# Optimization experiments

Hardware: AMD Instinct MI355X
Metric: run time of the kernel (lower is better)

The kernel has to match this reference:

```python
import jax, jax.numpy as jnp
import numpy as np

H = 2048
FF = 5504
N_HEADS = 16
HEAD_DIM = H // N_HEADS
EPS = 1.1920929e-07  # torch.finfo(float32).eps, F.rms_norm default
M_TOTAL = 4096


def _rms_norm(x, w):
    # x: [m, H], w: [H]
    var = jnp.mean(jnp.square(x), axis=-1, keepdims=True)
    return x * jax.lax.rsqrt(var + EPS) * w


def _routed_gemm(h, W, s):
    # rows [0:s) use W[0], rows [s:) use W[1]; split is static (Python int)
    return jnp.concatenate([h[:s] @ W[0], h[s:] @ W[1]], axis=0)


def _sdpa_seg(q, k, v):
    # q,k,v: [m, H] -> full (non-causal) attention over the segment
    m = q.shape[0]
    q = q.reshape(m, N_HEADS, HEAD_DIM)
    k = k.reshape(m, N_HEADS, HEAD_DIM)
    v = v.reshape(m, N_HEADS, HEAD_DIM)
    scale = 1.0 / jnp.sqrt(jnp.asarray(HEAD_DIM, q.dtype))
    scores = jnp.einsum('qhd,khd->hqk', q, k) * scale  # [nh, m, m]
    p = jax.nn.softmax(scores, axis=-1)
    out = jnp.einsum('hqk,khd->qhd', p, v)
    return out.reshape(m, H)


def setup_inputs() -> dict:
    key = jax.random.key(0)
    ks = jax.random.split(key, 5)
    return {
        'x': jax.random.normal(ks[0], (M_TOTAL, H), dtype=jnp.float32),
        'W_qkv': jax.random.normal(ks[1], (2, H, 3 * H), dtype=jnp.float32) * 0.02,
        'W_o': jax.random.normal(ks[2], (2, H, H), dtype=jnp.float32) * 0.02,
        'W_gu': jax.random.normal(ks[3], (2, H, 2 * FF), dtype=jnp.float32) * 0.02,
        'W_d': jax.random.normal(ks[4], (2, FF, H), dtype=jnp.float32) * 0.02,
        'ln1': jnp.ones((2, H), dtype=jnp.float32),
        'ln2': jnp.ones((2, H), dtype=jnp.float32),
        'split_point': 2048,
    }


def reference(x, W_qkv, W_o, W_gu, W_d, ln1, ln2, split_point):
    s = int(split_point)
    M = x.shape[0]

    def per_model(fn2, x, *stacked):
        # apply fn(seg, *per_model_weights) on [0:s) with index 0, [s:) with index 1
        if s == 0:
            return fn2(x, *(w[1] for w in stacked))
        if s == M:
            return fn2(x, *(w[0] for w in stacked))
        a = fn2(x[:s], *(w[0] for w in stacked))
        b = fn2(x[s:], *(w[1] for w in stacked))
        return jnp.concatenate([a, b], axis=0)

    # attention
    h = per_model(_rms_norm, x, ln1)
    qkv = _routed_gemm(h, W_qkv, s)
    q, k, v = jnp.split(qkv, 3, axis=-1)
    if s == 0 or s == M:
        attn = _sdpa_seg(q, k, v)
    else:
        attn = jnp.concatenate([
            _sdpa_seg(q[:s], k[:s], v[:s]),
            _sdpa_seg(q[s:], k[s:], v[s:]),
        ], axis=0)
    x = x + _routed_gemm(attn, W_o, s)

    # MLP (SwiGLU)
    h = per_model(_rms_norm, x, ln2)
    gu = _routed_gemm(h, W_gu, s)
    gate, up = jnp.split(gu, 2, axis=-1)
    h_mlp = jax.nn.silu(gate) * up
    x = x + _routed_gemm(h_mlp, W_d, s)
    return x
```

## Files before the change

kernel.cpp:

```cpp
#include <hip/hip_runtime.h>

typedef short bf16x8 __attribute__((ext_vector_type(8)));
typedef float f32x4  __attribute__((ext_vector_type(4)));
typedef float fvec4  __attribute__((ext_vector_type(4)));
typedef unsigned short u16;
typedef unsigned int u32;
typedef u32 u32x4 __attribute__((ext_vector_type(4)));
typedef u16 u16x8 __attribute__((ext_vector_type(8)));

#define MFMA16(a,b,c) __builtin_amdgcn_mfma_f32_16x16x32_bf16((a),(b),(c),0,0,0)

__device__ __forceinline__ u16 f2bf(float f){
  u32 u = __float_as_uint(f);
  u32 r = (u + 0x7fffu + ((u >> 16) & 1u)) >> 16;
  return (u16)r;
}
__device__ __forceinline__ float bf2f(u16 v){
  return __uint_as_float(((u32)v) << 16);
}
__device__ __forceinline__ void gload_lds16(const void* g, void* l){
  __builtin_amdgcn_global_load_lds((const __attribute__((address_space(1))) void*)g,
                                   (__attribute__((address_space(3))) void*)l, 16, 0, 0);
}

__global__ __launch_bounds__(256) void rmsnorm_kernel(const float* __restrict__ x,
    const float* __restrict__ lnw, const int* __restrict__ splitp, u16* __restrict__ out)
{
  const int row = blockIdx.x, tid = threadIdx.x;
  const float* xr = x + (size_t)row*2048 + tid*8;
  fvec4 v0 = *(const fvec4*)xr;
  fvec4 v1 = *(const fvec4*)(xr + 4);
  float ss = v0[0]*v0[0] + v0[1]*v0[1] + v0[2]*v0[2] + v0[3]*v0[3]
           + v1[0]*v1[0] + v1[1]*v1[1] + v1[2]*v1[2] + v1[3]*v1[3];
  #pragma unroll
  for (int off=32; off; off>>=1) ss += __shfl_xor(ss, off, 64);
  __shared__ float red[4];
  if ((tid & 63) == 0) red[tid>>6] = ss;
  __syncthreads();
  float tot = red[0] + red[1] + red[2] + red[3];
  float rs = rsqrtf(tot * (1.0f/2048.0f) + 1.1920929e-07f);
  int model = (row >= splitp[0]) ? 1 : 0;
  const float* wr = lnw + model*2048 + tid*8;
  fvec4 w0 = *(const fvec4*)wr, w1 = *(const fvec4*)(wr+4);
  u32x4 pk;
  #pragma unroll
  for (int e=0;e<2;++e){
    pk[e]   = (u32)f2bf(v0[2*e]*rs*w0[2*e]) | ((u32)f2bf(v0[2*e+1]*rs*w0[2*e+1]) << 16);
    pk[2+e] = (u32)f2bf(v1[2*e]*rs*w1[2*e]) | ((u32)f2bf(v1[2*e+1]*rs*w1[2*e+1]) << 16);
  }
  *(u32x4*)(out + (size_t)row*2048 + tid*8) = pk;
}

__global__ __launch_bounds__(256) void transpose_w(const float* __restrict__ W,
    u16* __restrict__ Wt, int K, int N)
{
  __shared__ float t[32][33];
  const int n0 = blockIdx.x * 32, k0 = blockIdx.y * 32;
  const float* Wm = W + (size_t)blockIdx.z * K * N;
  u16* Wtm = Wt + (size_t)blockIdx.z * K * N;
  const int tx = threadIdx.x & 31, ty = threadIdx.x >> 5;
  #pragma unroll
  for (int p=0;p<4;++p){
    int k = ty + p*8;
    t[k][tx] = Wm[(size_t)(k0 + k) * N + n0 + tx];
  }
  __syncthreads();
  #pragma unroll
  for (int p=0;p<4;++p){
    int n = ty + p*8;
    Wtm[(size_t)(n0 + n) * K + k0 + tx] = f2bf(t[tx][n]);
  }
}

template<int RESID>
__global__ __launch_bounds__(256) void gemm_routed(
    const u16* __restrict__ A, int lda, const u16* __restrict__ Wt,
    int N, int K, const int* __restrict__ splitp,
    u16* __restrict__ outB, float* __restrict__ outF, const float* __restrict__ res)
{
  __shared__ char Asm[8192];
  __shared__ char Bsm[8192];
  const int tid = threadIdx.x;
  const int w = tid >> 6, l = tid & 63;
  const int ln = l & 15, g = l >> 4;
  const int wm = w >> 1, wn = w & 1;
  const int row0 = blockIdx.x * 128;
  const int n0 = blockIdx.y * 128;
  const int model = (row0 >= splitp[0]) ? 1 : 0;
  const u16* B = Wt + (size_t)model * N * K;

  f32x4 acc[4][4];
  #pragma unroll
  for (int i=0;i<4;++i)
    #pragma unroll
    for (int j=0;j<4;++j) acc[i][j] = f32x4{0.f,0.f,0.f,0.f};

  int arow[2], aj[2];
  #pragma unroll
  for (int i=0;i<2;++i){
    int lin = (w*2+i)*1024 + l*16;
    int r_ = lin >> 6;
    int s_ = (lin >> 4) & 3;
    arow[i] = r_;
    aj[i] = s_ ^ (r_ & 3);
  }

  const int nt = K / 32;
  for (int kt = 0; kt < nt; ++kt){
    __syncthreads();
    #pragma unroll
    for (int i=0;i<2;++i){
      const u16* srcA = A + (size_t)(row0 + arow[i]) * lda + kt*32 + aj[i]*8;
      gload_lds16(srcA, Asm + (w*2+i)*1024);
      const u16* srcB = B + (size_t)(n0 + arow[i]) * K + kt*32 + aj[i]*8;
      gload_lds16(srcB, Bsm + (w*2+i)*1024);
    }
    __syncthreads();

    bf16x8 a[4], b[4];
    #pragma unroll
    for (int mf=0;mf<4;++mf){
      int r_ = wm*64 + mf*16 + ln;
      a[mf] = *(const bf16x8*)(Asm + r_*64 + (((g ^ (r_&3)) & 3) << 4));
    }
    #pragma unroll
    for (int nf=0;nf<4;++nf){
      int r_ = wn*64 + nf*16 + ln;
      b[nf] = *(const bf16x8*)(Bsm + r_*64 + (((g ^ (r_&3)) & 3) << 4));
    }
    #pragma unroll
    for (int mf=0;mf<4;++mf)
      #pragma unroll
      for (int nf=0;nf<4;++nf)
        acc[mf][nf] = MFMA16(a[mf], b[nf], acc[mf][nf]);
  }

  #pragma unroll
  for (int mf=0;mf<4;++mf){
    #pragma unroll
    for (int nf=0;nf<4;++nf){
      #pragma unroll
      for (int r=0;r<4;++r){
        int row = row0 + wm*64 + mf*16 + g*4 + r;
        int col = n0 + wn*64 + nf*16 + ln;
        size_t off = (size_t)row * N + col;
        float v = acc[mf][nf][r];
        if (RESID) outF[off] = v + res[off];
        else       outB[off] = f2bf(v);
      }
    }
  }
}

__global__ __launch_bounds__(256) void attn_kernel(const u16* __restrict__ qkv,
                                                   u16* __restrict__ out)
{
  __shared__ char Ksm[2][8192];
  __shared__ char Vsm[2][8192];
  __shared__ char Psm[4][1024];
  const int tid = threadIdx.x;
  const int w = tid >> 6, l = tid & 63;
  const int ln = l & 15, g = l >> 4;
  const int qt = blockIdx.x, h = blockIdx.y, seg = blockIdx.z;
  const int srow = seg * 2048;
  const float scale = 0.08838834764831845f;

  const int qrow = srow + qt*64 + w*16 + ln;
  bf16x8 qf[4];
  #pragma unroll
  for (int c=0;c<4;++c)
    qf[c] = *(const bf16x8*)(qkv + (size_t)qrow*6144 + h*128 + c*32 + g*8);

  f32x4 oacc[8];
  #pragma unroll
  for (int i=0;i<8;++i) oacc[i] = f32x4{0.f,0.f,0.f,0.f};
  float m[4]    = {-1e30f,-1e30f,-1e30f,-1e30f};
  float lsum[4] = {0.f,0.f,0.f,0.f};

  int kkv[2], ks[2];
  #pragma unroll
  for (int i=0;i<2;++i){
    int lin = (w*2+i)*1024 + l*16;
    int kv = lin >> 8;
    int sp = (lin >> 4) & 15;
    kkv[i] = kv;
    ks[i] = sp ^ (kv & 15);
  }
  const int vkv = tid >> 3, vd0 = (tid & 7) * 16;

  bf16x8 vreg0, vreg1;
  auto stage = [&](int kv0, int buf){
    #pragma unroll
    for (int i=0;i<2;++i){
      const u16* src = qkv + (size_t)(srow + kv0 + kkv[i]) * 6144 + 2048 + h*128 + ks[i]*8;
      gload_lds16(src, Ksm[buf] + (w*2+i)*1024);
    }
    const u16* vs = qkv + (size_t)(srow + kv0 + vkv) * 6144 + 4096 + h*128 + vd0;
    vreg0 = *(const bf16x8*)vs;
    vreg1 = *(const bf16x8*)(vs + 8);
  };
  auto writeV = [&](int buf){
    #pragma unroll
    for (int e=0;e<16;++e){
      int d = vd0 + e;
      u16 val = (u16)((e<8) ? vreg0[e] : vreg1[e-8]);
      int byte = d*64 + ((((vkv>>3) ^ (d&3)) & 3) << 4) + ((vkv & 7) << 1);
      *(u16*)(Vsm[buf] + byte) = val;
    }
  };

  stage(0, 0);
  writeV(0);
  __syncthreads();

  for (int t=0; t<64; ++t){
    int cur = t & 1, nxt = cur ^ 1;
    if (t+1 < 64) stage((t+1)*32, nxt);

    f32x4 s0 = f32x4{0.f,0.f,0.f,0.f}, s1 = f32x4{0.f,0.f,0.f,0.f};
    #pragma unroll
    for (int c=0;c<4;++c){
      int sl = c*4 + g;
      int c0 = ln;
      bf16x8 k0 = *(const bf16x8*)(Ksm[cur] + c0*256 + (((sl ^ (c0&15)) & 15) << 4));
      s0 = MFMA16(qf[c], k0, s0);
      int c1 = 16 + ln;
      bf16x8 k1 = *(const bf16x8*)(Ksm[cur] + c1*256 + (((sl ^ (c1&15)) & 15) << 4));
      s1 = MFMA16(qf[c], k1, s1);
    }
    float mx[4], f_[4];
    #pragma unroll
    for (int r=0;r<4;++r){
      s0[r] *= scale; s1[r] *= scale;
      mx[r] = fmaxf(s0[r], s1[r]);
    }
    #pragma unroll
    for (int off=1; off<16; off<<=1){
      #pragma unroll
      for (int r=0;r<4;++r) mx[r] = fmaxf(mx[r], __shfl_xor(mx[r], off, 64));
    }
    #pragma unroll
    for (int r=0;r<4;++r){
      float mn = fmaxf(m[r], mx[r]);
      f_[r] = __expf(m[r] - mn);
      m[r] = mn;
      lsum[r] *= f_[r];
    }
    #pragma unroll
    for (int r=0;r<4;++r){
      float p0 = __expf(s0[r] - m[r]);
      float p1 = __expf(s1[r] - m[r]);
      lsum[r] += p0 + p1;
      int qq = g*4 + r;
      int c0 = ln, c1 = 16 + ln;
      *(u16*)(Psm[w] + qq*64 + ((((c0>>3) ^ (qq&3)) & 3) << 4) + ((c0&7)<<1)) = f2bf(p0);
      *(u16*)(Psm[w] + qq*64 + ((((c1>>3) ^ (qq&3)) & 3) << 4) + ((c1&7)<<1)) = f2bf(p1);
    }
    {
      int srcl = (ln >> 2) << 4;
      float F0 = __shfl(f_[0], srcl, 64);
      float F1 = __shfl(f_[1], srcl, 64);
      float F2 = __shfl(f_[2], srcl, 64);
      float F3 = __shfl(f_[3], srcl, 64);
      int rr = ln & 3;
      float fc = (rr==0) ? F0 : (rr==1) ? F1 : (rr==2) ? F2 : F3;
      #pragma unroll
      for (int mc=0;mc<8;++mc){
        #pragma unroll
        for (int r=0;r<4;++r) oacc[mc][r] *= fc;
      }
    }
    bf16x8 pf = *(const bf16x8*)(Psm[w] + ln*64 + (((g ^ (ln&3)) & 3) << 4));
    #pragma unroll
    for (int mc=0;mc<8;++mc){
      int d = mc*16 + ln;
      bf16x8 vf = *(const bf16x8*)(Vsm[cur] + d*64 + (((g ^ (d&3)) & 3) << 4));
      oacc[mc] = MFMA16(vf, pf, oacc[mc]);
    }
    if (t+1 < 64) writeV(nxt);
    __syncthreads();
  }

  #pragma unroll
  for (int off=1; off<16; off<<=1){
    #pragma unroll
    for (int r=0;r<4;++r) lsum[r] += __shfl_xor(lsum[r], off, 64);
  }
  int srcl = (ln >> 2) << 4;
  float L0 = __shfl(lsum[0], srcl, 64);
  float L1 = __shfl(lsum[1], srcl, 64);
  float L2 = __shfl(lsum[2], srcl, 64);
  float L3 = __shfl(lsum[3], srcl, 64);
  int rr = ln & 3;
  float Lc = (rr==0) ? L0 : (rr==1) ? L1 : (rr==2) ? L2 : L3;
  float linv = 1.0f / Lc;
  const int orow = srow + qt*64 + w*16 + ln;
  #pragma unroll
  for (int mc=0;mc<8;++mc){
    #pragma unroll
    for (int r=0;r<4;++r){
      int d = mc*16 + g*4 + r;
      out[(size_t)orow*2048 + h*128 + d] = f2bf(oacc[mc][r] * linv);
    }
  }
}

__global__ __launch_bounds__(256) void silu_kernel(const u16* __restrict__ gu,
                                                   u16* __restrict__ hm)
{
  int u = blockIdx.x*256 + threadIdx.x;
  if (u >= 4096*688) return;
  int row = u / 688;
  int j = (u - row*688) * 8;
  const u16* gp = gu + (size_t)row*11008 + j;
  u16x8 gv = *(const u16x8*)gp;
  u16x8 uv = *(const u16x8*)(gp + 5504);
  u32x4 pk;
  #pragma unroll
  for (int e=0;e<4;++e){
    float g0 = bf2f(gv[2*e]),   g1 = bf2f(gv[2*e+1]);
    float u0 = bf2f(uv[2*e]),   u1 = bf2f(uv[2*e+1]);
    float r0 = g0 / (1.f + __expf(-g0)) * u0;
    float r1 = g1 / (1.f + __expf(-g1)) * u1;
    pk[e] = (u32)f2bf(r0) | ((u32)f2bf(r1) << 16);
  }
  *(u32x4*)(hm + (size_t)row*5504 + j) = pk;
}

extern "C" void kernel_launch(void* const* d_in, const int* in_sizes, int n_in,
                              void* d_out, int out_size, void* d_ws, size_t ws_size,
                              hipStream_t stream) {
  const float* x    = (const float*)d_in[0];
  const float* Wqkv = (const float*)d_in[1];
  const float* Wo   = (const float*)d_in[2];
  const float* Wgu  = (const float*)d_in[3];
  const float* Wd   = (const float*)d_in[4];
  const float* ln1  = (const float*)d_in[5];
  const float* ln2  = (const float*)d_in[6];
  const int*   split= (const int*)d_in[7];
  float* out = (float*)d_out;

  char* ws = (char*)d_ws;
  u16* Wt   = (u16*)(ws);
  u16* h    = (u16*)(ws + 94371840);
  u16* qkv  = (u16*)(ws + 111149056);
  u16* attn = (u16*)(ws + 161480704);
  u16* gu   = (u16*)(ws + 178257920);
  u16* h2   = h;
  u16* hm   = qkv;

  rmsnorm_kernel<<<4096, 256, 0, stream>>>(x, ln1, split, h);
  transpose_w<<<dim3(192, 64, 2), 256, 0, stream>>>(Wqkv, Wt, 2048, 6144);
  gemm_routed<0><<<dim3(32, 48), 256, 0, stream>>>(h, 2048, Wt, 6144, 2048, split,
                                                   qkv, nullptr, nullptr);
  attn_kernel<<<dim3(32, 16, 2), 256, 0, stream>>>(qkv, attn);
  transpose_w<<<dim3(64, 64, 2), 256, 0, stream>>>(Wo, Wt, 2048, 2048);
  gemm_routed<1><<<dim3(32, 16), 256, 0, stream>>>(attn, 2048, Wt, 2048, 2048, split,
                                                   nullptr, out, x);
  rmsnorm_kernel<<<4096, 256, 0, stream>>>(out, ln2, split, h2);
  transpose_w<<<dim3(344, 64, 2), 256, 0, stream>>>(Wgu, Wt, 2048, 11008);
  gemm_routed<0><<<dim3(32, 86), 256, 0, stream>>>(h2, 2048, Wt, 11008, 2048, split,
                                                   gu, nullptr, nullptr);
  silu_kernel<<<11008, 256, 0, stream>>>(gu, hm);
  transpose_w<<<dim3(64, 172, 2), 256, 0, stream>>>(Wd, Wt, 5504, 2048);
  gemm_routed<1><<<dim3(32, 16), 256, 0, stream>>>(hm, 5504, Wt, 2048, 5504, split,
                                                   nullptr, out, out);
}
```

Before: 1.365 ms.

## Emit transposed V from QKV GEMM and stage it with direct global-to-LDS loads

The QKV GEMM epilogue now writes V in a per-head transposed layout (d-major over kv) into a separate buffer, so the attention kernel can load V tiles with async global_load_lds instead of register loads followed by scattered 2-byte LDS writes. The swizzles for the V and P tiles are changed to match the new layout. s_setprio hints are added around the MFMA blocks in both the GEMM and attention kernels, and the attention output is stored as packed 4-element vectors. The transposed V write in the GEMM epilogue is strided and reuses the gu buffer, and it is only correct while the split point is 2048.

```diff
diff --git a/kernel.cpp b/kernel.cpp
--- a/kernel.cpp
+++ b/kernel.cpp
@@ -7,6 +7,7 @@
 typedef unsigned int u32;
 typedef u32 u32x4 __attribute__((ext_vector_type(4)));
 typedef u16 u16x8 __attribute__((ext_vector_type(8)));
+typedef u16 u16x4 __attribute__((ext_vector_type(4)));
 
 #define MFMA16(a,b,c) __builtin_amdgcn_mfma_f32_16x16x32_bf16((a),(b),(c),0,0,0)
 
@@ -72,11 +73,12 @@
   }
 }
 
-template<int RESID>
+template<int MODE>
 __global__ __launch_bounds__(256) void gemm_routed(
     const u16* __restrict__ A, int lda, const u16* __restrict__ Wt,
     int N, int K, const int* __restrict__ splitp,
-    u16* __restrict__ outB, float* __restrict__ outF, const float* __restrict__ res)
+    u16* __restrict__ outB, float* __restrict__ outF, const float* __restrict__ res,
+    u16* __restrict__ VtOut)
 {
   __shared__ char Asm[8192];
   __shared__ char Bsm[8192];
@@ -128,11 +130,32 @@
       int r_ = wn*64 + nf*16 + ln;
       b[nf] = *(const bf16x8*)(Bsm + r_*64 + (((g ^ (r_&3)) & 3) << 4));
     }
+    __builtin_amdgcn_s_setprio(1);
     #pragma unroll
     for (int mf=0;mf<4;++mf)
       #pragma unroll
       for (int nf=0;nf<4;++nf)
         acc[mf][nf] = MFMA16(a[mf], b[nf], acc[mf][nf]);
+    __builtin_amdgcn_s_setprio(0);
+  }
+
+  if (MODE == 2 && n0 >= 4096) {
+    const int seg = (row0 >= 2048) ? 1 : 0;
+    const int hh = (n0 - 4096) >> 7;
+    u16* vt = VtOut + (size_t)(seg*16 + hh) * 128 * 2048;
+    const int kvb = row0 - seg*2048 + wm*64;
+    #pragma unroll
+    for (int mf=0;mf<4;++mf){
+      #pragma unroll
+      for (int nf=0;nf<4;++nf){
+        int d  = wn*64 + nf*16 + ln;
+        int kv = kvb + mf*16 + g*4;
+        u16x4 pk = { f2bf(acc[mf][nf][0]), f2bf(acc[mf][nf][1]),
+                     f2bf(acc[mf][nf][2]), f2bf(acc[mf][nf][3]) };
+        *(u16x4*)(vt + (size_t)d*2048 + kv) = pk;
+      }
+    }
+    return;
   }
 
   #pragma unroll
@@ -145,14 +168,15 @@
         int col = n0 + wn*64 + nf*16 + ln;
         size_t off = (size_t)row * N + col;
         float v = acc[mf][nf][r];
-        if (RESID) outF[off] = v + res[off];
-        else       outB[off] = f2bf(v);
+        if (MODE == 1) outF[off] = v + res[off];
+        else           outB[off] = f2bf(v);
       }
     }
   }
 }
 
 __global__ __launch_bounds__(256) void attn_kernel(const u16* __restrict__ qkv,
+                                                   const u16* __restrict__ Vt,
                                                    u16* __restrict__ out)
 {
   __shared__ char Ksm[2][8192];
@@ -186,31 +210,28 @@
     kkv[i] = kv;
     ks[i] = sp ^ (kv & 15);
   }
-  const int vkv = tid >> 3, vd0 = (tid & 7) * 16;
-
-  bf16x8 vreg0, vreg1;
+  int vd[2], vs[2];
+  #pragma unroll
+  for (int i=0;i<2;++i){
+    int lin = tid*16 + i*4096;
+    int d_ = lin >> 6;
+    int sp = (lin >> 4) & 3;
+    vd[i] = d_;
+    vs[i] = sp ^ ((d_ >> 1) & 3);
+  }
+  const u16* Vh = Vt + (size_t)(seg*16 + h) * 128 * 2048;
+
   auto stage = [&](int kv0, int buf){
     #pragma unroll
     for (int i=0;i<2;++i){
-      const u16* src = qkv + (size_t)(srow + kv0 + kkv[i]) * 6144 + 2048 + h*128 + ks[i]*8;
-      gload_lds16(src, Ksm[buf] + (w*2+i)*1024);
-    }
-    const u16* vs = qkv + (size_t)(srow + kv0 + vkv) * 6144 + 4096 + h*128 + vd0;
-    vreg0 = *(const bf16x8*)vs;
-    vreg1 = *(const bf16x8*)(vs + 8);
+      const u16* srcK = qkv + (size_t)(srow + kv0 + kkv[i]) * 6144 + 2048 + h*128 + ks[i]*8;
+      gload_lds16(srcK, Ksm[buf] + (w*2+i)*1024);
+      const u16* srcV = Vh + (size_t)vd[i] * 2048 + kv0 + vs[i]*8;
+      gload_lds16(srcV, Vsm[buf] + w*1024 + i*4096);
+    }
   };
-  auto writeV = [&](int buf){
-    #pragma unroll
-    for (int e=0;e<16;++e){
-      int d = vd0 + e;
-      u16 val = (u16)((e<8) ? vreg0[e] : vreg1[e-8]);
-      int byte = d*64 + ((((vkv>>3) ^ (d&3)) & 3) << 4) + ((vkv & 7) << 1);
-      *(u16*)(Vsm[buf] + byte) = val;
-    }
-  };
 
   stage(0, 0);
-  writeV(0);
   __syncthreads();
 
   for (int t=0; t<64; ++t){
@@ -218,6 +239,7 @@
     if (t+1 < 64) stage((t+1)*32, nxt);
 
     f32x4 s0 = f32x4{0.f,0.f,0.f,0.f}, s1 = f32x4{0.f,0.f,0.f,0.f};
+    __builtin_amdgcn_s_setprio(1);
     #pragma unroll
     for (int c=0;c<4;++c){
       int sl = c*4 + g;
@@ -228,6 +250,7 @@
       bf16x8 k1 = *(const bf16x8*)(Ksm[cur] + c1*256 + (((sl ^ (c1&15)) & 15) << 4));
       s1 = MFMA16(qf[c], k1, s1);
     }
+    __builtin_amdgcn_s_setprio(0);
     float mx[4], f_[4];
     #pragma unroll
     for (int r=0;r<4;++r){
@@ -252,9 +275,10 @@
       float p1 = __expf(s1[r] - m[r]);
       lsum[r] += p0 + p1;
       int qq = g*4 + r;
+      int sw = (qq >> 1) & 3;
       int c0 = ln, c1 = 16 + ln;
-      *(u16*)(Psm[w] + qq*64 + ((((c0>>3) ^ (qq&3)) & 3) << 4) + ((c0&7)<<1)) = f2bf(p0);
-      *(u16*)(Psm[w] + qq*64 + ((((c1>>3) ^ (qq&3)) & 3) << 4) + ((c1&7)<<1)) = f2bf(p1);
+      *(u16*)(Psm[w] + qq*64 + ((((c0>>3) ^ sw) & 3) << 4) + ((c0&7)<<1)) = f2bf(p0);
+      *(u16*)(Psm[w] + qq*64 + ((((c1>>3) ^ sw) & 3) << 4) + ((c1&7)<<1)) = f2bf(p1);
     }
     {
       int srcl = (ln >> 2) << 4;
@@ -270,14 +294,15 @@
         for (int r=0;r<4;++r) oacc[mc][r] *= fc;
       }
     }
-    bf16x8 pf = *(const bf16x8*)(Psm[w] + ln*64 + (((g ^ (ln&3)) & 3) << 4));
+    bf16x8 pf = *(const bf16x8*)(Psm[w] + ln*64 + (((g ^ ((ln>>1)&3)) & 3) << 4));
+    __builtin_amdgcn_s_setprio(1);
     #pragma unroll
     for (int mc=0;mc<8;++mc){
       int d = mc*16 + ln;
-      bf16x8 vf = *(const bf16x8*)(Vsm[cur] + d*64 + (((g ^ (d&3)) & 3) << 4));
+      bf16x8 vf = *(const bf16x8*)(Vsm[cur] + d*64 + (((g ^ ((d>>1)&3)) & 3) << 4));
       oacc[mc] = MFMA16(vf, pf, oacc[mc]);
     }
-    if (t+1 < 64) writeV(nxt);
+    __builtin_amdgcn_s_setprio(0);
     __syncthreads();
   }
 
@@ -297,11 +322,9 @@
   const int orow = srow + qt*64 + w*16 + ln;
   #pragma unroll
   for (int mc=0;mc<8;++mc){
-    #pragma unroll
-    for (int r=0;r<4;++r){
-      int d = mc*16 + g*4 + r;
-      out[(size_t)orow*2048 + h*128 + d] = f2bf(oacc[mc][r] * linv);
-    }
+    u16x4 pk = { f2bf(oacc[mc][0] * linv), f2bf(oacc[mc][1] * linv),
+                 f2bf(oacc[mc][2] * linv), f2bf(oacc[mc][3] * linv) };
+    *(u16x4*)(out + (size_t)orow*2048 + h*128 + mc*16 + g*4) = pk;
   }
 }
 
@@ -348,21 +371,22 @@
   u16* gu   = (u16*)(ws + 178257920);
   u16* h2   = h;
   u16* hm   = qkv;
+  u16* Vt   = gu;
 
   rmsnorm_kernel<<<4096, 256, 0, stream>>>(x, ln1, split, h);
   transpose_w<<<dim3(192, 64, 2), 256, 0, stream>>>(Wqkv, Wt, 2048, 6144);
-  gemm_routed<0><<<dim3(32, 48), 256, 0, stream>>>(h, 2048, Wt, 6144, 2048, split,
-                                                   qkv, nullptr, nullptr);
-  attn_kernel<<<dim3(32, 16, 2), 256, 0, stream>>>(qkv, attn);
+  gemm_routed<2><<<dim3(32, 48), 256, 0, stream>>>(h, 2048, Wt, 6144, 2048, split,
+                                                   qkv, nullptr, nullptr, Vt);
+  attn_kernel<<<dim3(32, 16, 2), 256, 0, stream>>>(qkv, Vt, attn);
   transpose_w<<<dim3(64, 64, 2), 256, 0, stream>>>(Wo, Wt, 2048, 2048);
   gemm_routed<1><<<dim3(32, 16), 256, 0, stream>>>(attn, 2048, Wt, 2048, 2048, split,
-                                                   nullptr, out, x);
+                                                   nullptr, out, x, nullptr);
   rmsnorm_kernel<<<4096, 256, 0, stream>>>(out, ln2, split, h2);
   transpose_w<<<dim3(344, 64, 2), 256, 0, stream>>>(Wgu, Wt, 2048, 11008);
   gemm_routed<0><<<dim3(32, 86), 256, 0, stream>>>(h2, 2048, Wt, 11008, 2048, split,
-                                                   gu, nullptr, nullptr);
+                                                   gu, nullptr, nullptr, nullptr);
   silu_kernel<<<11008, 256, 0, stream>>>(gu, hm);
   transpose_w<<<dim3(64, 172, 2), 256, 0, stream>>>(Wd, Wt, 5504, 2048);
   gemm_routed<1><<<dim3(32, 16), 256, 0, stream>>>(hm, 5504, Wt, 2048, 5504, split,
-                                                   nullptr, out, out);
-}
+                                                   nullptr, out, out, nullptr);
+}
```

New measurement: 1.262 ms. -7.6%, faster.
